# Kernel optimization log

Hardware: AMD Instinct MI355X
Metric: run time of the kernel (lower is better)

The kernel has to match this reference:

```python
import jax, jax.numpy as jnp
import numpy as np
from jax import lax

# Ring of the 8 non-center positions of a 3x3 kernel, cyclic clockwise
# starting at top-middle. A rotation offset 'off' (in 1/8 turns) shifts
# kernel taps around this ring; 'off' = step*rot where step = 8/kernel_rot.
_RING = [(0, 1), (0, 2), (1, 2), (2, 2), (2, 1), (2, 0), (1, 0), (0, 0)]
_CENTER = (1, 1)


def _tap_positions(kernel_type, off):
    """Return list of (row, col) 3x3 positions, one per stored kernel value."""
    if kernel_type == 0:  # skel: 5 taps = 4-point cross (rotated) + center
        pos = [_RING[(2 * k + off) % 8] for k in range(4)] + [_CENTER]
    elif kernel_type == 1:  # full 3x3: 8 ring taps (rotated) + center
        pos = [_RING[(k + off) % 8] for k in range(8)] + [_CENTER]
    else:  # bar: tap - center - opposite tap, rotated
        pos = [_RING[off % 8], _CENTER, _RING[(4 + off) % 8]]
    return pos


def _build_dense_kernel(weight, kernel_type, off):
    # weight: [O, I, num_kernel] -> dense [O, I, 3, 3]
    O, I, nk = weight.shape
    dense = jnp.zeros((O, I, 3, 3), dtype=weight.dtype)
    for k, (r, c) in enumerate(_tap_positions(kernel_type, off)):
        dense = dense.at[:, :, r, c].set(weight[:, :, k])
    return dense


def setup_inputs() -> dict:
    key = jax.random.key(0)
    k1, k2 = jax.random.split(key)
    x_tensor = jax.random.normal(k1, (16, 64, 192, 192), dtype=jnp.float32)
    weight = jax.random.normal(k2, (64, 64, 5), dtype=jnp.float32) * 0.05
    return {"x_tensor": x_tensor, "weight": weight, "rot": 1}


def reference(x_tensor, weight, rot):
    kernel_type = 0          # skel
    kernel_rot = 8
    step = 8 // kernel_rot   # = 1
    off = (step * int(rot)) % 8
    dense = _build_dense_kernel(weight, kernel_type, off)  # [O, I, 3, 3]
    # 3x3 conv, stride 1, padding 1, dilation 1, NCHW/OIHW
    out = lax.conv_general_dilated(
        x_tensor, dense,
        window_strides=(1, 1),
        padding=[(1, 1), (1, 1)],
        rhs_dilation=(1, 1),
        dimension_numbers=("NCHW", "OIHW", "NCHW"),
    )
    return out
```

## Files before the change

kernel.cpp:

```cpp
#include <hip/hip_runtime.h>

#define WD   192
#define HD   192
#define HWD  (WD*HD)
#define NCH  64
#define NOUT 64
#define NK   5
#define BAND 6
#define COLS 194
#define ROWB 128

typedef __attribute__((ext_vector_type(8))) short short8;
typedef __attribute__((ext_vector_type(4))) float f32x4;

__device__ inline ushort f2bf(float f) {
  union { float f; unsigned u; } xx; xx.f = f;
  unsigned u = xx.u;
  return (ushort)((u + 0x7FFFu + ((u >> 16) & 1u)) >> 16);
}

__device__ inline int ldso(int slot, int pix, int cbyte) {
  int byte = (slot * COLS + pix) * ROWB + cbyte;
  return byte ^ ((pix & 7) << 4);
}

__global__ void prep_taps_k(const int* __restrict__ rot, int* __restrict__ taps) {
  const int ring_r[8] = {0,0,1,2,2,2,1,0};
  const int ring_c[8] = {1,2,2,2,1,0,0,0};
  int off = ((rot[0] % 8) + 8) % 8;
  for (int k = 0; k < 4; ++k) {
    int p = (2*k + off) & 7;
    taps[k] = 0; taps[5 + k] = ring_r[p] - 1; taps[10 + k] = ring_c[p] - 1;
  }
  taps[4] = 0; taps[9] = 0; taps[14] = 0;
}

__device__ inline unsigned s3(int gr) { return (unsigned)(gr + 3) % 3u; }

__device__ inline void lds_barrier() {
  __builtin_amdgcn_sched_barrier(0);
  asm volatile("s_waitcnt lgkmcnt(0)" ::: "memory");
  __builtin_amdgcn_sched_barrier(0);
  __builtin_amdgcn_s_barrier();
  __builtin_amdgcn_sched_barrier(0);
}

__global__ __launch_bounds__(512, 2) void rconv_ring_k(
    const float* __restrict__ x, const float* __restrict__ w,
    const int* __restrict__ taps, float* __restrict__ out) {
  __shared__ ushort lds[3 * COLS * (ROWB / 2)];
  char* ldsb = (char*)lds;

  const int tid  = threadIdx.x;
  const int lane = tid & 63;
  const int wv   = tid >> 6;
  const int l15  = lane & 15;
  const int g    = lane >> 4;
  const int r0   = blockIdx.x * BAND;
  const int n    = blockIdx.y;
  const int o0w  = (wv & 1) * 32;
  const int wq   = wv >> 1;

  int dr[NK], dc[NK];
  #pragma unroll
  for (int k = 0; k < NK; ++k) { dr[k] = taps[5 + k]; dc[k] = taps[10 + k]; }

  short8 a[2][2][NK];
  #pragma unroll
  for (int ot = 0; ot < 2; ++ot)
    #pragma unroll
    for (int kc = 0; kc < 2; ++kc)
      #pragma unroll
      for (int k = 0; k < NK; ++k) {
        short8 t;
        #pragma unroll
        for (int j = 0; j < 8; ++j)
          t[j] = (short)f2bf(w[(size_t)(o0w + ot*16 + l15) * (NCH*NK)
                               + (kc*32 + g*8 + j) * NK + k]);
        a[ot][kc][k] = t;
      }

  const float* xn = x + ((size_t)n * NCH + wv * 8) * HWD;

  auto stage_load = [&](int gr, float v[3][8]) {
    bool vr = (gr >= 0) && (gr < HD);
    if (vr) {
      const float* xr = xn + (size_t)gr * WD;
      #pragma unroll
      for (int i = 0; i < 3; ++i)
        #pragma unroll
        for (int j = 0; j < 8; ++j)
          v[i][j] = xr[(size_t)j * HWD + i * 64 + lane];
    } else {
      #pragma unroll
      for (int i = 0; i < 3; ++i)
        #pragma unroll
        for (int j = 0; j < 8; ++j) v[i][j] = 0.f;
    }
  };
  auto stage_write = [&](int gr, const float v[3][8]) {
    int s = s3(gr);
    #pragma unroll
    for (int i = 0; i < 3; ++i) {
      short8 t;
      #pragma unroll
      for (int j = 0; j < 8; ++j) t[j] = (short)f2bf(v[i][j]);
      *reinterpret_cast<short8*>(ldsb + ldso(s, 1 + i * 64 + lane, wv * 16)) = t;
    }
    if (lane < 2) {
      short8 z = (short8){0,0,0,0,0,0,0,0};
      *reinterpret_cast<short8*>(ldsb + ldso(s, lane * (COLS - 1), wv * 16)) = z;
    }
  };

  f32x4 acc[3][2];
  auto compute_row = [&](int r) {
    int bo0[NK], bo1[NK];
    #pragma unroll
    for (int k = 0; k < NK; ++k) {
      int pix = wq * 48 + dc[k] + 1 + l15;
      bo0[k] = ldso(s3(r + dr[k]), pix, g * 16);
      bo1[k] = ldso(s3(r + dr[k]), pix, g * 16 + 64);
    }
    #pragma unroll
    for (int t = 0; t < 3; ++t) {
      acc[t][0] = (f32x4){0.f, 0.f, 0.f, 0.f};
      acc[t][1] = (f32x4){0.f, 0.f, 0.f, 0.f};
    }
    __builtin_amdgcn_s_setprio(1);
    #pragma unroll
    for (int t = 0; t < 3; ++t)
      #pragma unroll
      for (int k = 0; k < NK; ++k) {
        short8 b0 = *reinterpret_cast<const short8*>(ldsb + bo0[k] + t * 16 * ROWB);
        short8 b1 = *reinterpret_cast<const short8*>(ldsb + bo1[k] + t * 16 * ROWB);
        acc[t][0] = __builtin_amdgcn_mfma_f32_16x16x32_bf16(a[0][0][k], b0, acc[t][0], 0, 0, 0);
        acc[t][1] = __builtin_amdgcn_mfma_f32_16x16x32_bf16(a[1][0][k], b0, acc[t][1], 0, 0, 0);
        acc[t][0] = __builtin_amdgcn_mfma_f32_16x16x32_bf16(a[0][1][k], b1, acc[t][0], 0, 0, 0);
        acc[t][1] = __builtin_amdgcn_mfma_f32_16x16x32_bf16(a[1][1][k], b1, acc[t][1], 0, 0, 0);
      }
    __builtin_amdgcn_s_setprio(0);
  };
  auto store_row = [&](int r) {
    size_t ob = ((size_t)(n * NOUT + o0w + 4 * g) * HD + r) * WD + wq * 48 + l15;
    #pragma unroll
    for (int t = 0; t < 3; ++t)
      #pragma unroll
      for (int ot = 0; ot < 2; ++ot)
        #pragma unroll
        for (int q = 0; q < 4; ++q)
          out[ob + (size_t)(ot * 16 + q) * HWD + t * 16] = acc[t][ot][q];
  };

  float v[3][8];

  stage_load(r0 - 1, v); stage_write(r0 - 1, v);
  stage_load(r0,     v); stage_write(r0,     v);
  stage_load(r0 + 1, v); stage_write(r0 + 1, v);
  __syncthreads();

  #pragma unroll 1
  for (int r = r0; r < r0 + BAND; ++r) {
    const bool do_stage = (r + 2 <= r0 + BAND);
    if (do_stage) stage_load(r + 2, v);
    compute_row(r);
    lds_barrier();
    if (do_stage) stage_write(r + 2, v);
    lds_barrier();
    store_row(r);
  }
}

extern "C" void kernel_launch(void* const* d_in, const int* in_sizes, int n_in,
                              void* d_out, int out_size, void* d_ws, size_t ws_size,
                              hipStream_t stream) {
  const float* x = (const float*)d_in[0];
  const float* w = (const float*)d_in[1];
  const int* rot = (const int*)d_in[2];
  float* out     = (float*)d_out;
  int* taps      = (int*)d_ws;

  const int nbatch = in_sizes[0] / (NCH * HWD);

  hipLaunchKernelGGL(prep_taps_k, dim3(1), dim3(1), 0, stream, rot, taps);
  hipLaunchKernelGGL(rconv_ring_k, dim3(HD / BAND, nbatch), dim3(512), 0, stream,
                     x, w, taps, out);
}
```

Baseline: 89.90 us.

## Deepen row pipeline to six LDS slots and compute two rows per barrier

Grows the LDS ring buffer from three to six row slots and doubles the band height per block. Each phase now converts two prefetched rows, issues global loads for rows further ahead, computes two output rows, and writes the staged rows, with one barrier per two rows instead of two per row. The aim is to hide global load latency better and cut synchronisation overhead. In exchange it doubles LDS use and holds more registers for prefetch and accumulators, which may lower occupancy. Larger bands also halve the grid size.

```diff
diff --git a/kernel.cpp b/kernel.cpp
--- a/kernel.cpp
+++ b/kernel.cpp
@@ -6,7 +6,8 @@
 #define NCH  64
 #define NOUT 64
 #define NK   5
-#define BAND 6
+#define BAND 12
+#define SLOTS 6
 #define COLS 194
 #define ROWB 128
 
@@ -35,7 +36,7 @@
   taps[4] = 0; taps[9] = 0; taps[14] = 0;
 }
 
-__device__ inline unsigned s3(int gr) { return (unsigned)(gr + 3) % 3u; }
+__device__ inline unsigned s6(int gr) { return (unsigned)(gr + 6) % 6u; }
 
 __device__ inline void lds_barrier() {
   __builtin_amdgcn_sched_barrier(0);
@@ -48,7 +49,7 @@
 __global__ __launch_bounds__(512, 2) void rconv_ring_k(
     const float* __restrict__ x, const float* __restrict__ w,
     const int* __restrict__ taps, float* __restrict__ out) {
-  __shared__ ushort lds[3 * COLS * (ROWB / 2)];
+  __shared__ ushort lds[SLOTS * COLS * (ROWB / 2)];
   char* ldsb = (char*)lds;
 
   const int tid  = threadIdx.x;
@@ -98,29 +99,33 @@
         for (int j = 0; j < 8; ++j) v[i][j] = 0.f;
     }
   };
-  auto stage_write = [&](int gr, const float v[3][8]) {
-    int s = s3(gr);
+  auto cvt_row = [&](const float v[3][8], short8 c[3]) {
     #pragma unroll
     for (int i = 0; i < 3; ++i) {
       short8 t;
       #pragma unroll
       for (int j = 0; j < 8; ++j) t[j] = (short)f2bf(v[i][j]);
-      *reinterpret_cast<short8*>(ldsb + ldso(s, 1 + i * 64 + lane, wv * 16)) = t;
-    }
+      c[i] = t;
+    }
+  };
+  auto stage_write_bf = [&](int gr, const short8 c[3]) {
+    int s = s6(gr);
+    #pragma unroll
+    for (int i = 0; i < 3; ++i)
+      *reinterpret_cast<short8*>(ldsb + ldso(s, 1 + i * 64 + lane, wv * 16)) = c[i];
     if (lane < 2) {
       short8 z = (short8){0,0,0,0,0,0,0,0};
       *reinterpret_cast<short8*>(ldsb + ldso(s, lane * (COLS - 1), wv * 16)) = z;
     }
   };
 
-  f32x4 acc[3][2];
-  auto compute_row = [&](int r) {
+  auto compute_row = [&](int r, f32x4 acc[3][2]) {
     int bo0[NK], bo1[NK];
     #pragma unroll
     for (int k = 0; k < NK; ++k) {
       int pix = wq * 48 + dc[k] + 1 + l15;
-      bo0[k] = ldso(s3(r + dr[k]), pix, g * 16);
-      bo1[k] = ldso(s3(r + dr[k]), pix, g * 16 + 64);
+      bo0[k] = ldso(s6(r + dr[k]), pix, g * 16);
+      bo1[k] = ldso(s6(r + dr[k]), pix, g * 16 + 64);
     }
     #pragma unroll
     for (int t = 0; t < 3; ++t) {
@@ -141,7 +146,7 @@
       }
     __builtin_amdgcn_s_setprio(0);
   };
-  auto store_row = [&](int r) {
+  auto store_row = [&](int r, const f32x4 acc[3][2]) {
     size_t ob = ((size_t)(n * NOUT + o0w + 4 * g) * HD + r) * WD + wq * 48 + l15;
     #pragma unroll
     for (int t = 0; t < 3; ++t)
@@ -152,22 +157,41 @@
           out[ob + (size_t)(ot * 16 + q) * HWD + t * 16] = acc[t][ot][q];
   };
 
-  float v[3][8];
-
-  stage_load(r0 - 1, v); stage_write(r0 - 1, v);
-  stage_load(r0,     v); stage_write(r0,     v);
-  stage_load(r0 + 1, v); stage_write(r0 + 1, v);
+  float vA0[3][8], vA1[3][8], vB0[3][8], vB1[3][8];
+  f32x4 accA[3][2], accB[3][2];
+
+  {
+    short8 c[3];
+    stage_load(r0 - 1, vA0); stage_load(r0, vA1);
+    cvt_row(vA0, c); stage_write_bf(r0 - 1, c);
+    cvt_row(vA1, c); stage_write_bf(r0,     c);
+    stage_load(r0 + 1, vA0); stage_load(r0 + 2, vA1);
+    cvt_row(vA0, c); stage_write_bf(r0 + 1, c);
+    cvt_row(vA1, c); stage_write_bf(r0 + 2, c);
+    stage_load(r0 + 3, vA0); stage_load(r0 + 4, vA1);
+  }
   __syncthreads();
 
+  auto phase = [&](int r, float (&s0)[3][8], float (&s1)[3][8],
+                   float (&d0)[3][8], float (&d1)[3][8]) {
+    const bool gw = (r + 3 <= r0 + BAND);
+    const bool gl = (r + 5 <= r0 + BAND);
+    short8 c0[3], c1[3];
+    if (gw) { cvt_row(s0, c0); cvt_row(s1, c1); }
+    if (gl) { stage_load(r + 5, d0); stage_load(r + 6, d1); }
+    compute_row(r,     accA);
+    compute_row(r + 1, accB);
+    if (gw) { stage_write_bf(r + 3, c0); stage_write_bf(r + 4, c1); }
+    lds_barrier();
+    store_row(r,     accA);
+    store_row(r + 1, accB);
+  };
+
   #pragma unroll 1
-  for (int r = r0; r < r0 + BAND; ++r) {
-    const bool do_stage = (r + 2 <= r0 + BAND);
-    if (do_stage) stage_load(r + 2, v);
-    compute_row(r);
-    lds_barrier();
-    if (do_stage) stage_write(r + 2, v);
-    lds_barrier();
-    store_row(r);
+  for (int ii = 0; ii < BAND / 4; ++ii) {
+    int r = r0 + 4 * ii;
+    phase(r,     vA0, vA1, vB0, vB1);
+    phase(r + 2, vB0, vB1, vA0, vA1);
   }
 }
 
```

Result: slower. 290.4 us (+223.1%).

## Process two rows per iteration with a six-slot LDS ring and fewer barriers

Applied to the files above, without the earlier changes.

Doubles the row band per block from 6 to 12 and grows the LDS row ring from 3 to 6 slots. The main loop now computes two output rows per iteration and stages the next two input rows. It needs only one barrier per pair of rows instead of two per row, and it cuts halo reloads per block. In exchange, LDS use grows to about 149KB per block, so likely only one block fits per CU. The grid also halves to 256 blocks, and register pressure rises from the doubled staging buffers and accumulators.

```diff
diff --git a/kernel.cpp b/kernel.cpp
--- a/kernel.cpp
+++ b/kernel.cpp
@@ -6,7 +6,8 @@
 #define NCH  64
 #define NOUT 64
 #define NK   5
-#define BAND 6
+#define BAND 12
+#define SLOTS 6
 #define COLS 194
 #define ROWB 128
 
@@ -35,7 +36,7 @@
   taps[4] = 0; taps[9] = 0; taps[14] = 0;
 }
 
-__device__ inline unsigned s3(int gr) { return (unsigned)(gr + 3) % 3u; }
+__device__ inline unsigned s6(int gr) { return (unsigned)(gr + 6) % 6u; }
 
 __device__ inline void lds_barrier() {
   __builtin_amdgcn_sched_barrier(0);
@@ -45,11 +46,51 @@
   __builtin_amdgcn_sched_barrier(0);
 }
 
+#define COMPUTE_ROW(rr, acc) do {                                              \
+  int bo0[NK], bo1[NK];                                                        \
+  _Pragma("unroll")                                                            \
+  for (int k = 0; k < NK; ++k) {                                               \
+    int pix = wq * 48 + dc[k] + 1 + l15;                                       \
+    bo0[k] = ldso(s6((rr) + dr[k]), pix, g * 16);                              \
+    bo1[k] = ldso(s6((rr) + dr[k]), pix, g * 16 + 64);         \
+  }                                                                            \
+  _Pragma("unroll")                                                            \
+  for (int t = 0; t < 3; ++t) { acc[t][0] = zf; acc[t][1] = zf; }              \
+  __builtin_amdgcn_s_setprio(1);                                               \
+  _Pragma("unroll")                                                            \
+  for (int t = 0; t < 3; ++t) {                                                \
+    _Pragma("unroll")                                                          \
+    for (int k = 0; k < NK; ++k) {                                             \
+      short8 b0 = *reinterpret_cast<const short8*>(ldsb + bo0[k] + t*16*ROWB); \
+      short8 b1 = *reinterpret_cast<const short8*>(ldsb + bo1[k] + t*16*ROWB); \
+      acc[t][0] = __builtin_amdgcn_mfma_f32_16x16x32_bf16(a[0][0][k], b0, acc[t][0], 0, 0, 0); \
+      acc[t][1] = __builtin_amdgcn_mfma_f32_16x16x32_bf16(a[1][0][k], b0, acc[t][1], 0, 0, 0); \
+      acc[t][0] = __builtin_amdgcn_mfma_f32_16x16x32_bf16(a[0][1][k], b1, acc[t][0], 0, 0, 0); \
+      acc[t][1] = __builtin_amdgcn_mfma_f32_16x16x32_bf16(a[1][1][k], b1, acc[t][1], 0, 0, 0); \
+    }                                                                          \
+  }                                                                            \
+  __builtin_amdgcn_s_setprio(0);                                               \
+} while (0)
+
+#define STORE_ROW(rr, acc) do {                                                \
+  size_t ob = ((size_t)(n * NOUT + o0w + 4 * g) * HD + (rr)) * WD + wq*48 + l15; \
+  _Pragma("unroll")                                                            \
+  for (int t = 0; t < 3; ++t) {                                                \
+    _Pragma("unroll")                                                          \
+    for (int ot = 0; ot < 2; ++ot) {                                           \
+      _Pragma("unroll")                                                        \
+      for (int q = 0; q < 4; ++q)                                              \
+        out[ob + (size_t)(ot*16 + q) * HWD + t*16] = acc[t][ot][q];            \
+    }                                                                          \
+  }                                                                            \
+} while (0)
+
 __global__ __launch_bounds__(512, 2) void rconv_ring_k(
     const float* __restrict__ x, const float* __restrict__ w,
     const int* __restrict__ taps, float* __restrict__ out) {
-  __shared__ ushort lds[3 * COLS * (ROWB / 2)];
+  __shared__ ushort lds[SLOTS * COLS * (ROWB / 2)];
   char* ldsb = (char*)lds;
+  const f32x4 zf = (f32x4){0.f, 0.f, 0.f, 0.f};
 
   const int tid  = threadIdx.x;
   const int lane = tid & 63;
@@ -99,7 +140,7 @@
     }
   };
   auto stage_write = [&](int gr, const float v[3][8]) {
-    int s = s3(gr);
+    int s = s6(gr);
     #pragma unroll
     for (int i = 0; i < 3; ++i) {
       short8 t;
@@ -113,61 +154,26 @@
     }
   };
 
-  f32x4 acc[3][2];
-  auto compute_row = [&](int r) {
-    int bo0[NK], bo1[NK];
-    #pragma unroll
-    for (int k = 0; k < NK; ++k) {
-      int pix = wq * 48 + dc[k] + 1 + l15;
-      bo0[k] = ldso(s3(r + dr[k]), pix, g * 16);
-      bo1[k] = ldso(s3(r + dr[k]), pix, g * 16 + 64);
-    }
-    #pragma unroll
-    for (int t = 0; t < 3; ++t) {
-      acc[t][0] = (f32x4){0.f, 0.f, 0.f, 0.f};
-      acc[t][1] = (f32x4){0.f, 0.f, 0.f, 0.f};
-    }
-    __builtin_amdgcn_s_setprio(1);
-    #pragma unroll
-    for (int t = 0; t < 3; ++t)
-      #pragma unroll
-      for (int k = 0; k < NK; ++k) {
-        short8 b0 = *reinterpret_cast<const short8*>(ldsb + bo0[k] + t * 16 * ROWB);
-        short8 b1 = *reinterpret_cast<const short8*>(ldsb + bo1[k] + t * 16 * ROWB);
-        acc[t][0] = __builtin_amdgcn_mfma_f32_16x16x32_bf16(a[0][0][k], b0, acc[t][0], 0, 0, 0);
-        acc[t][1] = __builtin_amdgcn_mfma_f32_16x16x32_bf16(a[1][0][k], b0, acc[t][1], 0, 0, 0);
-        acc[t][0] = __builtin_amdgcn_mfma_f32_16x16x32_bf16(a[0][1][k], b1, acc[t][0], 0, 0, 0);
-        acc[t][1] = __builtin_amdgcn_mfma_f32_16x16x32_bf16(a[1][1][k], b1, acc[t][1], 0, 0, 0);
-      }
-    __builtin_amdgcn_s_setprio(0);
-  };
-  auto store_row = [&](int r) {
-    size_t ob = ((size_t)(n * NOUT + o0w + 4 * g) * HD + r) * WD + wq * 48 + l15;
-    #pragma unroll
-    for (int t = 0; t < 3; ++t)
-      #pragma unroll
-      for (int ot = 0; ot < 2; ++ot)
-        #pragma unroll
-        for (int q = 0; q < 4; ++q)
-          out[ob + (size_t)(ot * 16 + q) * HWD + t * 16] = acc[t][ot][q];
-  };
+  float vA[3][8], vB[3][8];
+  f32x4 accA[3][2], accB[3][2];
 
-  float v[3][8];
-
-  stage_load(r0 - 1, v); stage_write(r0 - 1, v);
-  stage_load(r0,     v); stage_write(r0,     v);
-  stage_load(r0 + 1, v); stage_write(r0 + 1, v);
+  stage_load(r0 - 1, vA); stage_write(r0 - 1, vA);
+  stage_load(r0,     vA); stage_write(r0,     vA);
+  stage_load(r0 + 1, vA); stage_write(r0 + 1, vA);
+  stage_load(r0 + 2, vA); stage_write(r0 + 2, vA);
   __syncthreads();
 
   #pragma unroll 1
-  for (int r = r0; r < r0 + BAND; ++r) {
-    const bool do_stage = (r + 2 <= r0 + BAND);
-    if (do_stage) stage_load(r + 2, v);
-    compute_row(r);
+  for (int p = 0; p < BAND / 2; ++p) {
+    int r = r0 + 2 * p;
+    const bool gl = (r + 3 <= r0 + BAND);
+    if (gl) { stage_load(r + 3, vA); stage_load(r + 4, vB); }
+    COMPUTE_ROW(r,     accA);
+    COMPUTE_ROW(r + 1, accB);
+    if (gl) { stage_write(r + 3, vA); stage_write(r + 4, vB); }
     lds_barrier();
-    if (do_stage) stage_write(r + 2, v);
-    lds_barrier();
-    store_row(r);
+    STORE_ROW(r,     accA);
+    STORE_ROW(r + 1, accB);
   }
 }
 
```

Result: slower. 96.61 us (+7.5%).
